# Performance work log

Hardware: AMD Instinct MI355X
Metric: run time of the kernel (lower is better)

## Reference

```python
import jax, jax.numpy as jnp
import numpy as np

C = 512
GROUPS = 32
EPS = 1e-6


def setup_inputs() -> dict:
    key = jax.random.key(0)
    ks = jax.random.split(key, 10)
    b, c, w = 8, C, 2048
    scale = 1.0 / np.sqrt(c)
    inp = {
        "x": jax.random.normal(ks[0], (b, c, w), dtype=jnp.float32),
        "gn_gamma": jnp.ones((c,), dtype=jnp.float32),
        "gn_beta": jnp.zeros((c,), dtype=jnp.float32),
        "wq": jax.random.normal(ks[1], (c, c), dtype=jnp.float32) * scale,
        "bq": jnp.zeros((c,), dtype=jnp.float32),
        "wk": jax.random.normal(ks[2], (c, c), dtype=jnp.float32) * scale,
        "bk": jnp.zeros((c,), dtype=jnp.float32),
        "wv": jax.random.normal(ks[3], (c, c), dtype=jnp.float32) * scale,
        "bv": jnp.zeros((c,), dtype=jnp.float32),
        "wp": jax.random.normal(ks[4], (c, c), dtype=jnp.float32) * scale,
        "bp": jnp.zeros((c,), dtype=jnp.float32),
    }
    return inp


def _group_norm(x, gamma, beta):
    # x: (b, c, w) -> normalize over (c//G, w) within each of G groups
    b, c, w = x.shape
    xg = x.reshape(b, GROUPS, c // GROUPS, w)
    mean = jnp.mean(xg, axis=(2, 3), keepdims=True)
    var = jnp.var(xg, axis=(2, 3), keepdims=True)
    xg = (xg - mean) * jax.lax.rsqrt(var + EPS)
    xn = xg.reshape(b, c, w)
    return xn * gamma[None, :, None] + beta[None, :, None]


def reference(x, gn_gamma, gn_beta, wq, bq, wk, bk, wv, bv, wp, bp):
    b, c, w = x.shape
    h = _group_norm(x, gn_gamma, gn_beta)
    # 1x1 convs == per-position linear over channels
    q = jnp.einsum('oc,bcw->bow', wq, h) + bq[None, :, None]
    k = jnp.einsum('oc,bcw->bow', wk, h) + bk[None, :, None]
    v = jnp.einsum('oc,bcw->bow', wv, h) + bv[None, :, None]
    # scores[b, i, j] = sum_c q[b,c,i] * k[b,c,j]
    scores = jnp.einsum('bci,bcj->bij', q, k) * (float(c) ** -0.5)
    att = jax.nn.softmax(scores, axis=2)  # (b, w, w)
    # out[b,c,i] = sum_j v[b,c,j] * att[b,i,j]
    h = jnp.einsum('bcj,bij->bci', v, att)
    h = jnp.einsum('oc,bcw->bow', wp, h) + bp[None, :, None]
    return x + h
```

## Files before the change

kernel.cpp:

```cpp
#include <hip/hip_runtime.h>
#include <hip/hip_bf16.h>
#include <stdint.h>

#define CDIM 512
#define WDIM 2048
#define BDIM 8
#define NGRP 32
#define LOG2E 1.4426950408889634f

typedef unsigned short u16;
typedef unsigned char u8;
typedef __attribute__((ext_vector_type(8))) short bf16x8;
typedef __attribute__((ext_vector_type(4))) float f32x4;
typedef __attribute__((ext_vector_type(2))) long long2v;

__device__ __forceinline__ float bf2f(u16 u) {
  return __builtin_bit_cast(float, (uint32_t)(u) << 16);
}
__device__ __forceinline__ u16 f2bf(float f) {
  return __builtin_bit_cast(u16, __float2bfloat16(f));
}
__device__ __forceinline__ u8 f2f8(float f) {
  return (u8)(__builtin_amdgcn_cvt_pk_fp8_f32(f, 0.f, 0, false));
}

__device__ __forceinline__ void gld_lds16(const void* g, void* l) {
  __builtin_amdgcn_global_load_lds(
      (const __attribute__((address_space(1))) uint32_t*)(uintptr_t)(g),
      (__attribute__((address_space(3))) uint32_t*)(uintptr_t)(l),
      16, 0, 0);
}

__device__ __forceinline__ int pi64(int l) {
  return ((l >> 3) & 3) * 16 + ((l >> 5) & 1) * 8 + (l & 7);
}

__global__ __launch_bounds__(256) void cvt_weights(
    const float* __restrict__ a, const float* __restrict__ b,
    const float* __restrict__ c, const float* __restrict__ d,
    u16* __restrict__ o) {
  int i = blockIdx.x * 256 + threadIdx.x;
  o[i]          = f2bf(a[i]);
  o[262144 + i] = f2bf(b[i]);
  o[524288 + i] = f2bf(c[i]);
  o[786432 + i] = f2bf(d[i]);
}

__global__ __launch_bounds__(512) void gn_fused(
    const float* __restrict__ x, const float* __restrict__ gamma,
    const float* __restrict__ beta, u16* __restrict__ hT) {
  extern __shared__ u16 hbuf[];
  __shared__ float red[2][8];
  __shared__ float mrsh[2];
  const int bg = blockIdx.x;
  const int b = bg >> 5, g = bg & 31;
  const int tid = threadIdx.x;
  const float4* xp = (const float4*)(x + (size_t)bg * 16 * WDIM);
  float s = 0.f, s2 = 0.f;
  for (int i = tid; i < 16 * WDIM / 4; i += 512) {
    float4 v = xp[i];
    s += v.x + v.y + v.z + v.w;
    s2 = fmaf(v.x, v.x, s2); s2 = fmaf(v.y, v.y, s2);
    s2 = fmaf(v.z, v.z, s2); s2 = fmaf(v.w, v.w, s2);
    int e = i * 4;
    int cc = e >> 11, w = e & 2047;
    u16* p = &hbuf[cc * 2052 + w];
    p[0] = f2bf(v.x); p[1] = f2bf(v.y); p[2] = f2bf(v.z); p[3] = f2bf(v.w);
  }
  for (int off = 32; off; off >>= 1) {
    s  += __shfl_xor(s, off, 64);
    s2 += __shfl_xor(s2, off, 64);
  }
  if ((tid & 63) == 0) { red[0][tid >> 6] = s; red[1][tid >> 6] = s2; }
  __syncthreads();
  if (tid == 0) {
    float S = 0.f, S2 = 0.f;
    #pragma unroll
    for (int i = 0; i < 8; ++i) { S += red[0][i]; S2 += red[1][i]; }
    const float inv_n = 1.0f / (16.0f * WDIM);
    float m = S * inv_n;
    float var = S2 * inv_n - m * m;
    mrsh[0] = m; mrsh[1] = rsqrtf(var + 1e-6f);
  }
  __syncthreads();
  const float m = mrsh[0], r = mrsh[1];
  float ga[16], bb[16];
  #pragma unroll
  for (int cc = 0; cc < 16; ++cc) {
    float gm = gamma[g * 16 + cc] * r;
    ga[cc] = gm;
    bb[cc] = beta[g * 16 + cc] - m * gm;
  }
  #pragma unroll
  for (int rr = 0; rr < 4; ++rr) {
    int w = rr * 512 + tid;
    u16 ov[16];
    #pragma unroll
    for (int cc = 0; cc < 16; ++cc)
      ov[cc] = f2bf(fmaf(bf2f(hbuf[cc * 2052 + w]), ga[cc], bb[cc]));
    u16* dst = hT + ((size_t)b * WDIM + w) * CDIM + g * 16;
    *(uint4*)(dst)     = *(const uint4*)(&ov[0]);
    *(uint4*)(dst + 8) = *(const uint4*)(&ov[8]);
  }
}

__global__ __launch_bounds__(256) void sm_combine(
    const float* __restrict__ lpart, float* __restrict__ linv) {
  int idx = blockIdx.x * 256 + threadIdx.x;
  int b = idx >> 11, i = idx & 2047;
  float l = 0.f;
  #pragma unroll
  for (int p = 0; p < 8; ++p)
    l += lpart[((size_t)b * 8 + p) * 2048 + i];
  linv[idx] = 1.0f / l;
}

template <int BIAS_MODE, int RESID, int SCALE, typename OutT, int SMEXP>
__global__ __launch_bounds__(512, 1) void gemm_tn(
    const u16* __restrict__ A, const u16* __restrict__ B,
    OutT* __restrict__ Cp, const float* __restrict__ bias,
    const float* __restrict__ bias2, const float* __restrict__ resid,
    float* __restrict__ LP, float scale, int K, int N, int lda, int ldb,
    long sAb, long sBb, long sCb, int gx, int gy) {
  constexpr int BM_ = 128, BN_ = 256;
  constexpr int MI = 4;
  constexpr int CB = 2, L = 3;
  constexpr int ABYTES = BM_ * 64;
  constexpr int SLOT = (BM_ + BN_) * 64;
  extern __shared__ char smem[];
  const int tid = threadIdx.x;
  const int wave = tid >> 6, lane = tid & 63;
  const int wr = wave >> 2, wc = wave & 3;
  const int fr = lane & 15, kg = lane >> 4;

  const int nq = gridDim.x >> 3;
  const int sid = (blockIdx.x & 7) * nq + (blockIdx.x >> 3);
  const int bx = sid % gx;
  const int t1 = sid / gx;
  const int by = t1 % gy;
  const int bz = t1 / gy;

  const size_t zc = (size_t)bz * sCb;
  const u16* Ab = A + (size_t)bz * sAb + (size_t)bx * BM_ * lda;
  const u16* Bb = B + (size_t)bz * sBb + (size_t)by * BN_ * ldb;

  int aoff, boff[CB];
  {
    int pc = tid;
    int S = pc >> 3, p = (pc & 7) ^ (S & 7);
    aoff = (2 * S + (p >> 2)) * lda + (p & 3) * 8;
  }
  #pragma unroll
  for (int j = 0; j < CB; ++j) {
    int pc = j * 512 + tid;
    int S = pc >> 3, p = (pc & 7) ^ (S & 7);
    boff[j] = (2 * S + (p >> 2)) * ldb + (p & 3) * 8;
  }
  const int rbase = (fr >> 1) * 128 + (((((fr & 1) << 2) | kg) ^ (fr >> 1)) << 4);
  const int sAo = wr * 64 * 64;
  const int sBo = wc * 64 * 64;

  f32x4 acc[MI][4] = {};

  auto stage = [&](int buf, int tk) {
    char* d = smem + buf * SLOT;
    gld_lds16(Ab + aoff + tk * 32, d + tid * 16);
    #pragma unroll
    for (int j = 0; j < CB; ++j)
      gld_lds16(Bb + boff[j] + tk * 32, d + ABYTES + (j * 512 + tid) * 16);
  };

  const int nt = K >> 5;
  stage(0, 0);
  stage(1, 1);
  asm volatile("s_waitcnt vmcnt(%0)" :: "n"(L) : "memory");
  __builtin_amdgcn_s_barrier();

  for (int t = 0; t < nt; ++t) {
    const char* base = smem + (t % 3) * SLOT;
    const bool st = (t + 2 < nt);
    if (st) stage((t + 2) % 3, t + 2);
    bf16x8 af[4], bfv[4];
    #pragma unroll
    for (int i = 0; i < 4; ++i)
      af[i] = *(const bf16x8*)(base + sAo + i * 1024 + rbase);
    #pragma unroll
    for (int ni = 0; ni < 4; ++ni)
      bfv[ni] = *(const bf16x8*)(base + ABYTES + sBo + ni * 1024 + rbase);
    asm volatile("s_waitcnt lgkmcnt(0)" ::: "memory");
    __builtin_amdgcn_sched_barrier(0);
    __builtin_amdgcn_s_setprio(1);
    #pragma unroll
    for (int i = 0; i < 4; ++i)
      #pragma unroll
      for (int ni = 0; ni < 4; ++ni)
        acc[i][ni] = __builtin_amdgcn_mfma_f32_16x16x32_bf16(
            af[i], bfv[ni], acc[i][ni], 0, 0, 0);
    __builtin_amdgcn_s_setprio(0);
    if (st)
      asm volatile("s_waitcnt vmcnt(%0)" :: "n"(L) : "memory");
    else if (t + 1 < nt)
      asm volatile("s_waitcnt vmcnt(0)" ::: "memory");
    if (t + 1 < nt)
      __builtin_amdgcn_s_barrier();
  }

  float rs[MI][4];
  if constexpr (SMEXP) {
    #pragma unroll
    for (int mi = 0; mi < MI; ++mi)
      #pragma unroll
      for (int j = 0; j < 4; ++j) rs[mi][j] = 0.f;
  }

  const int row0 = bx * BM_ + wr * 64 + kg * 4;
  const int coln = by * BN_ + wc * 64 + fr;
  #pragma unroll
  for (int mi = 0; mi < MI; ++mi) {
    #pragma unroll
    for (int ni = 0; ni < 4; ++ni) {
      int n = coln + ni * 16;
      float badd = 0.0f;
      if (BIAS_MODE == 3) badd = (n < 512) ? bias[n] : bias2[n - 512];
      #pragma unroll
      for (int j = 0; j < 4; ++j) {
        int m = row0 + mi * 16 + j;
        float v = acc[mi][ni][j];
        if (BIAS_MODE == 2) v += bias[m];
        else if (BIAS_MODE == 3) v += badd;
        if (SCALE) v *= scale;
        if constexpr (SMEXP) {
          v = exp2f(v * LOG2E);
          rs[mi][j] += v;
        }
        if (BIAS_MODE == 4) v *= bias[(size_t)bz * 2048 + m];
        if constexpr (sizeof(OutT) == 1) {
          int l = n & 63;
          ((u8*)Cp)[zc + (size_t)m * N + (size_t)(n & ~63) + pi64(l)] = f2f8(v);
        } else {
          size_t idx = zc + (size_t)m * N + n;
          if (RESID) v += resid[idx];
          if constexpr (sizeof(OutT) == 2) {
            Cp[idx] = (OutT)f2bf(v);
          } else {
            Cp[idx] = v;
          }
        }
      }
    }
  }

  if constexpr (SMEXP) {
    float* redl = (float*)smem;
    __syncthreads();
    #pragma unroll
    for (int mi = 0; mi < MI; ++mi) {
      #pragma unroll
      for (int j = 0; j < 4; ++j) {
        float l = rs[mi][j];
        #pragma unroll
        for (int msk = 1; msk < 16; msk <<= 1)
          l += __shfl_xor(l, msk, 64);
        if (fr == 0) {
          int rr = wr * 64 + mi * 16 + kg * 4 + j;
          redl[rr * 4 + wc] = l;
        }
      }
    }
    __syncthreads();
    if (tid < 128) {
      float l = redl[tid * 4] + redl[tid * 4 + 1] +
                redl[tid * 4 + 2] + redl[tid * 4 + 3];
      LP[((size_t)bz * 8 + by) * 2048 + bx * 128 + tid] = l;
    }
  }
}

template <int BIAS_MODE, int SCALE, typename OutT, int SMEXP>
__global__ __launch_bounds__(512, 1) void gemm_f8(
    const u8* __restrict__ A, const u8* __restrict__ B,
    OutT* __restrict__ Cp, const float* __restrict__ bias,
    float* __restrict__ LP, float scale, int K, int N, int ldaB, int ldbB,
    long sAb, long sBb, long sCb, int gx, int gy) {
  constexpr int MI = 4;
  constexpr int CB = 2, L = 3;
  constexpr int ABYTES = 8192;
  constexpr int SLOT = 24576;
  extern __shared__ char smem[];
  const int tid = threadIdx.x;
  const int wave = tid >> 6, lane = tid & 63;
  const int wr = wave >> 2, wc = wave & 3;
  const int fr = lane & 15, kg = lane >> 4;

  const int nq = gridDim.x >> 3;
  const int sid = (blockIdx.x & 7) * nq + (blockIdx.x >> 3);
  const int bx = sid % gx;
  const int t1 = sid / gx;
  const int by = t1 % gy;
  const int bz = t1 / gy;

  const size_t zc = (size_t)bz * sCb;
  const u8* Ab = A + (size_t)bz * sAb + (size_t)bx * 128 * ldaB;
  const u8* Bb = B + (size_t)bz * sBb + (size_t)by * 256 * ldbB;

  int aoff, boff[CB];
  {
    int pc = tid;
    int S = pc >> 3, p = (pc & 7) ^ (S & 7);
    aoff = (2 * S + (p >> 2)) * ldaB + (p & 3) * 16;
  }
  #pragma unroll
  for (int j = 0; j < CB; ++j) {
    int pc = j * 512 + tid;
    int S = pc >> 3, p = (pc & 7) ^ (S & 7);
    boff[j] = (2 * S + (p >> 2)) * ldbB + (p & 3) * 16;
  }
  const int rbase = (fr >> 1) * 128 + (((((fr & 1) << 2) | kg) ^ (fr >> 1)) << 4);
  const int sAo = wr * 4096;
  const int sBo = wc * 4096;

  f32x4 acc[MI][4] = {};

  auto stage = [&](int buf, int tk) {
    char* d = smem + buf * SLOT;
    gld_lds16(Ab + aoff + tk * 64, d + tid * 16);
    #pragma unroll
    for (int j = 0; j < CB; ++j)
      gld_lds16(Bb + boff[j] + tk * 64, d + ABYTES + (j * 512 + tid) * 16);
  };

  const int nt = K >> 6;
  stage(0, 0);
  stage(1, 1);
  asm volatile("s_waitcnt vmcnt(%0)" :: "n"(L) : "memory");
  __builtin_amdgcn_s_barrier();

  for (int t = 0; t < nt; ++t) {
    const char* base = smem + (t % 3) * SLOT;
    const bool st = (t + 2 < nt);
    if (st) stage((t + 2) % 3, t + 2);
    long2v af[4], bfv[4];
    #pragma unroll
    for (int i = 0; i < 4; ++i)
      af[i] = *(const long2v*)(base + sAo + i * 1024 + rbase);
    #pragma unroll
    for (int ni = 0; ni < 4; ++ni)
      bfv[ni] = *(const long2v*)(base + ABYTES + sBo + ni * 1024 + rbase);
    asm volatile("s_waitcnt lgkmcnt(0)" ::: "memory");
    __builtin_amdgcn_sched_barrier(0);
    __builtin_amdgcn_s_setprio(1);
    #pragma unroll
    for (int ksl = 0; ksl < 2; ++ksl)
      #pragma unroll
      for (int i = 0; i < 4; ++i)
        #pragma unroll
        for (int ni = 0; ni < 4; ++ni)
          acc[i][ni] = __builtin_amdgcn_mfma_f32_16x16x32_fp8_fp8(
              af[i][ksl], bfv[ni][ksl], acc[i][ni], 0, 0, 0);
    __builtin_amdgcn_s_setprio(0);
    if (st)
      asm volatile("s_waitcnt vmcnt(%0)" :: "n"(L) : "memory");
    else if (t + 1 < nt)
      asm volatile("s_waitcnt vmcnt(0)" ::: "memory");
    if (t + 1 < nt)
      __builtin_amdgcn_s_barrier();
  }

  float rs[MI][4];
  if constexpr (SMEXP) {
    #pragma unroll
    for (int mi = 0; mi < MI; ++mi)
      #pragma unroll
      for (int j = 0; j < 4; ++j) rs[mi][j] = 0.f;
  }

  const int row0 = bx * 128 + wr * 64 + kg * 4;
  const int coln = by * 256 + wc * 64 + fr;
  #pragma unroll
  for (int mi = 0; mi < MI; ++mi) {
    #pragma unroll
    for (int ni = 0; ni < 4; ++ni) {
      int n = coln + ni * 16;
      #pragma unroll
      for (int j = 0; j < 4; ++j) {
        int m = row0 + mi * 16 + j;
        float v = acc[mi][ni][j];
        if (SCALE) v *= scale;
        if constexpr (SMEXP) {
          v = exp2f(fmaf(v, LOG2E, -4.0f));
          rs[mi][j] += v;
        }
        if (BIAS_MODE == 4) v *= bias[(size_t)bz * 2048 + m];
        if constexpr (sizeof(OutT) == 1) {
          int l = n & 63;
          ((u8*)Cp)[zc + (size_t)m * N + (size_t)(n & ~63) + pi64(l)] = f2f8(v);
        } else {
          Cp[zc + (size_t)m * N + n] = (OutT)f2bf(v);
        }
      }
    }
  }

  if constexpr (SMEXP) {
    float* redl = (float*)smem;
    __syncthreads();
    #pragma unroll
    for (int mi = 0; mi < MI; ++mi) {
      #pragma unroll
      for (int j = 0; j < 4; ++j) {
        float l = rs[mi][j];
        #pragma unroll
        for (int msk = 1; msk < 16; msk <<= 1)
          l += __shfl_xor(l, msk, 64);
        if (fr == 0) {
          int rr = wr * 64 + mi * 16 + kg * 4 + j;
          redl[rr * 4 + wc] = l;
        }
      }
    }
    __syncthreads();
    if (tid < 128) {
      float l = redl[tid * 4] + redl[tid * 4 + 1] +
                redl[tid * 4 + 2] + redl[tid * 4 + 3];
      LP[((size_t)bz * 8 + by) * 2048 + bx * 128 + tid] = l;
    }
  }
}

extern "C" void kernel_launch(void* const* d_in, const int* in_sizes, int n_in,
                              void* d_out, int out_size, void* d_ws,
                              size_t ws_size, hipStream_t stream) {
  const float* x     = (const float*)d_in[0];
  const float* gamma = (const float*)d_in[1];
  const float* beta  = (const float*)d_in[2];
  const float* wq    = (const float*)d_in[3];
  const float* bq    = (const float*)d_in[4];
  const float* wk    = (const float*)d_in[5];
  const float* bk    = (const float*)d_in[6];
  const float* wv    = (const float*)d_in[7];
  const float* bv    = (const float*)d_in[8];
  const float* wp    = (const float*)d_in[9];
  const float* bp    = (const float*)d_in[10];
  float* out = (float*)d_out;

  char* ws = (char*)d_ws;
  u16* wq_bf = (u16*)ws;
  u16* wv_bf = wq_bf + 524288;
  u16* wp_bf = wv_bf + 262144;
  u16* hT = (u16*)(ws + 4 * 524288);
  u8*  qk8 = (u8*)(hT + 8388608);
  u8*  vB8 = qk8 + 16777216;
  u16* oT  = (u16*)(vB8 + 8388608);
  u8*  sc8 = (u8*)(oT + 8388608);
  float* lpart = (float*)(sc8 + 33554432);
  float* linv  = lpart + 131072;

  const long sWC = (long)WDIM * CDIM;
  const long sCW = (long)CDIM * WDIM;
  const long sQK = (long)WDIM * 1024;
  const long sWW = (long)WDIM * WDIM;

  const int SMEM = 3 * (128 + 256) * 64;
  const int GN_SMEM = 16 * 2052 * 2;
  (void)hipFuncSetAttribute((const void*)&gn_fused,
      hipFuncAttributeMaxDynamicSharedMemorySize, GN_SMEM);
  (void)hipFuncSetAttribute((const void*)&gemm_tn<3, 0, 0, u8, 0>,
      hipFuncAttributeMaxDynamicSharedMemorySize, SMEM);
  (void)hipFuncSetAttribute((const void*)&gemm_tn<2, 0, 0, u8, 0>,
      hipFuncAttributeMaxDynamicSharedMemorySize, SMEM);
  (void)hipFuncSetAttribute((const void*)&gemm_f8<0, 1, u8, 1>,
      hipFuncAttributeMaxDynamicSharedMemorySize, SMEM);
  (void)hipFuncSetAttribute((const void*)&gemm_f8<4, 0, u16, 0>,
      hipFuncAttributeMaxDynamicSharedMemorySize, SMEM);
  (void)hipFuncSetAttribute((const void*)&gemm_tn<2, 1, 0, float, 0>,
      hipFuncAttributeMaxDynamicSharedMemorySize, SMEM);

  cvt_weights<<<1024, 256, 0, stream>>>(wq, wk, wv, wp, wq_bf);
  gn_fused<<<BDIM * NGRP, 512, GN_SMEM, stream>>>(x, gamma, beta, hT);

  const float scale = 0.04419417382415922f;

  gemm_tn<3, 0, 0, u8, 0><<<512, 512, SMEM, stream>>>(
      hT, wq_bf, qk8, bq, bk, nullptr, nullptr, 1.f, 512, 1024,
      512, 512, sWC, 0, sQK, 16, 4);
  gemm_tn<2, 0, 0, u8, 0><<<256, 512, SMEM, stream>>>(
      wv_bf, hT, vB8, bv, nullptr, nullptr, nullptr, 1.f, 512, 2048,
      512, 512, 0, sWC, sCW, 4, 8);
  gemm_f8<0, 1, u8, 1><<<1024, 512, SMEM, stream>>>(
      qk8, qk8 + 512, sc8, nullptr, lpart, scale, 512, 2048,
      1024, 1024, sQK, sQK, sWW, 16, 8);
  sm_combine<<<64, 256, 0, stream>>>(lpart, linv);
  gemm_f8<4, 0, u16, 0><<<256, 512, SMEM, stream>>>(
      sc8, vB8, oT, linv, nullptr, 1.f, 2048, 512,
      2048, 2048, sWW, sCW, sWC, 16, 2);
  gemm_tn<2, 1, 0, float, 0><<<256, 512, SMEM, stream>>>(
      wp_bf, oT, out, bp, nullptr, x, nullptr, 1.f, 512, 2048,
      512, 512, 0, sWC, sCW, 4, 8);
}
```

Measured before the change: 158.3 us.

## Switch QKV projections to FP8 MFMA with FP8 group-norm output

Group norm now writes its normalized activations directly as FP8 in the permuted 64-byte layout the FP8 GEMM expects. The Q/K and V weights are converted to FP8 in the same layout. The Q/K and V projection GEMMs then run on the FP8 GEMM kernel instead of the BF16 one. This halves activation and weight bytes and doubles MFMA k-depth per instruction for those GEMMs, at the cost of lower precision in Q, K and V. The weight conversion kernel is restructured to use fewer blocks, and the two GEMM templates are consolidated.

```diff
diff --git a/kernel.cpp b/kernel.cpp
--- a/kernel.cpp
+++ b/kernel.cpp
@@ -10,6 +10,7 @@
 
 typedef unsigned short u16;
 typedef unsigned char u8;
+typedef unsigned long long u64;
 typedef __attribute__((ext_vector_type(8))) short bf16x8;
 typedef __attribute__((ext_vector_type(4))) float f32x4;
 typedef __attribute__((ext_vector_type(2))) long long2v;
@@ -36,19 +37,43 @@
 }
 
 __global__ __launch_bounds__(256) void cvt_weights(
-    const float* __restrict__ a, const float* __restrict__ b,
-    const float* __restrict__ c, const float* __restrict__ d,
-    u16* __restrict__ o) {
-  int i = blockIdx.x * 256 + threadIdx.x;
-  o[i]          = f2bf(a[i]);
-  o[262144 + i] = f2bf(b[i]);
-  o[524288 + i] = f2bf(c[i]);
-  o[786432 + i] = f2bf(d[i]);
+    const float* __restrict__ wq, const float* __restrict__ wk,
+    const float* __restrict__ wv, const float* __restrict__ wp,
+    u8* __restrict__ wqk8, u8* __restrict__ wv8, u16* __restrict__ wp_bf) {
+  const int t = blockIdx.x * 256 + threadIdx.x;
+  if (t < 8192) {
+    int row = t >> 3, c0 = (t & 7) * 64;
+    const float* src = (row < 512) ? wq + (size_t)row * 512 + c0
+                                   : wk + (size_t)(row - 512) * 512 + c0;
+    u8 buf[64];
+    #pragma unroll
+    for (int l = 0; l < 64; ++l) buf[pi64(l)] = f2f8(src[l]);
+    u8* dst = wqk8 + (size_t)row * 512 + c0;
+    #pragma unroll
+    for (int q = 0; q < 4; ++q)
+      *(uint4*)(dst + q * 16) = *(const uint4*)(buf + q * 16);
+  } else if (t < 12288) {
+    int t2 = t - 8192;
+    int row = t2 >> 3, c0 = (t2 & 7) * 64;
+    const float* src = wv + (size_t)row * 512 + c0;
+    u8 buf[64];
+    #pragma unroll
+    for (int l = 0; l < 64; ++l) buf[pi64(l)] = f2f8(src[l]);
+    u8* dst = wv8 + (size_t)row * 512 + c0;
+    #pragma unroll
+    for (int q = 0; q < 4; ++q)
+      *(uint4*)(dst + q * 16) = *(const uint4*)(buf + q * 16);
+  }
+  #pragma unroll
+  for (int j = 0; j < 16; ++j) {
+    int i = t * 16 + j;
+    wp_bf[i] = f2bf(wp[i]);
+  }
 }
 
 __global__ __launch_bounds__(512) void gn_fused(
     const float* __restrict__ x, const float* __restrict__ gamma,
-    const float* __restrict__ beta, u16* __restrict__ hT) {
+    const float* __restrict__ beta, u8* __restrict__ h8) {
   extern __shared__ u16 hbuf[];
   __shared__ float red[2][8];
   __shared__ float mrsh[2];
@@ -91,42 +116,44 @@
     ga[cc] = gm;
     bb[cc] = beta[g * 16 + cc] - m * gm;
   }
+  const int gq = g & 3;
+  const int off0 = ((2 * gq) & 3) * 16 + (gq >> 1) * 8;
+  const int off1 = ((2 * gq + 1) & 3) * 16 + (gq >> 1) * 8;
   #pragma unroll
   for (int rr = 0; rr < 4; ++rr) {
     int w = rr * 512 + tid;
-    u16 ov[16];
+    u8 ov[16];
     #pragma unroll
     for (int cc = 0; cc < 16; ++cc)
-      ov[cc] = f2bf(fmaf(bf2f(hbuf[cc * 2052 + w]), ga[cc], bb[cc]));
-    u16* dst = hT + ((size_t)b * WDIM + w) * CDIM + g * 16;
-    *(uint4*)(dst)     = *(const uint4*)(&ov[0]);
-    *(uint4*)(dst + 8) = *(const uint4*)(&ov[8]);
-  }
-}
-
+      ov[cc] = f2f8(fmaf(bf2f(hbuf[cc * 2052 + w]), ga[cc], bb[cc]));
+    u8* dst = h8 + ((size_t)b * WDIM + w) * CDIM + (g >> 2) * 64;
+    *(u64*)(dst + off0) = *(const u64*)(&ov[0]);
+    *(u64*)(dst + off1) = *(const u64*)(&ov[8]);
+  }
+}
+
+template <int NP>
 __global__ __launch_bounds__(256) void sm_combine(
     const float* __restrict__ lpart, float* __restrict__ linv) {
   int idx = blockIdx.x * 256 + threadIdx.x;
   int b = idx >> 11, i = idx & 2047;
   float l = 0.f;
   #pragma unroll
-  for (int p = 0; p < 8; ++p)
-    l += lpart[((size_t)b * 8 + p) * 2048 + i];
+  for (int p = 0; p < NP; ++p)
+    l += lpart[((size_t)b * NP + p) * 2048 + i];
   linv[idx] = 1.0f / l;
 }
 
-template <int BIAS_MODE, int RESID, int SCALE, typename OutT, int SMEXP>
+template <int BIAS_MODE, int RESID, typename OutT>
 __global__ __launch_bounds__(512, 1) void gemm_tn(
     const u16* __restrict__ A, const u16* __restrict__ B,
     OutT* __restrict__ Cp, const float* __restrict__ bias,
-    const float* __restrict__ bias2, const float* __restrict__ resid,
-    float* __restrict__ LP, float scale, int K, int N, int lda, int ldb,
-    long sAb, long sBb, long sCb, int gx, int gy) {
-  constexpr int BM_ = 128, BN_ = 256;
+    const float* __restrict__ resid, float scale, int K, int N,
+    int lda, int ldb, long sAb, long sBb, long sCb, int gx, int gy) {
   constexpr int MI = 4;
   constexpr int CB = 2, L = 3;
-  constexpr int ABYTES = BM_ * 64;
-  constexpr int SLOT = (BM_ + BN_) * 64;
+  constexpr int ABYTES = 8192;
+  constexpr int SLOT = 24576;
   extern __shared__ char smem[];
   const int tid = threadIdx.x;
   const int wave = tid >> 6, lane = tid & 63;
@@ -141,8 +168,8 @@
   const int bz = t1 / gy;
 
   const size_t zc = (size_t)bz * sCb;
-  const u16* Ab = A + (size_t)bz * sAb + (size_t)bx * BM_ * lda;
-  const u16* Bb = B + (size_t)bz * sBb + (size_t)by * BN_ * ldb;
+  const u16* Ab = A + (size_t)bz * sAb + (size_t)bx * 128 * lda;
+  const u16* Bb = B + (size_t)bz * sBb + (size_t)by * 256 * ldb;
 
   int aoff, boff[CB];
   {
@@ -157,8 +184,8 @@
     boff[j] = (2 * S + (p >> 2)) * ldb + (p & 3) * 8;
   }
   const int rbase = (fr >> 1) * 128 + (((((fr & 1) << 2) | kg) ^ (fr >> 1)) << 4);
-  const int sAo = wr * 64 * 64;
-  const int sBo = wc * 64 * 64;
+  const int sAo = wr * 4096;
+  const int sBo = wc * 4096;
 
   f32x4 acc[MI][4] = {};
 
@@ -205,6 +232,122 @@
       __builtin_amdgcn_s_barrier();
   }
 
+  const int row0 = bx * 128 + wr * 64 + kg * 4;
+  const int coln = by * 256 + wc * 64 + fr;
+  #pragma unroll
+  for (int mi = 0; mi < MI; ++mi) {
+    #pragma unroll
+    for (int ni = 0; ni < 4; ++ni) {
+      int n = coln + ni * 16;
+      #pragma unroll
+      for (int j = 0; j < 4; ++j) {
+        int m = row0 + mi * 16 + j;
+        float v = acc[mi][ni][j];
+        if (BIAS_MODE == 2) v += bias[m];
+        size_t idx = zc + (size_t)m * N + n;
+        if (RESID) v += resid[idx];
+        if constexpr (sizeof(OutT) == 2) {
+          Cp[idx] = (OutT)f2bf(v);
+        } else {
+          Cp[idx] = v;
+        }
+      }
+    }
+  }
+  (void)scale;
+}
+
+template <int BIAS_MODE, int SCALE, typename OutT, int SMEXP>
+__global__ __launch_bounds__(512, 1) void gemm_f8(
+    const u8* __restrict__ A, const u8* __restrict__ B,
+    OutT* __restrict__ Cp, const float* __restrict__ bias,
+    const float* __restrict__ bias2, float* __restrict__ LP,
+    float scale, int K, int N, int ldaB, int ldbB,
+    long sAb, long sBb, long sCb, int gx, int gy) {
+  constexpr int MI = 4;
+  constexpr int CB = 2, L = 3;
+  constexpr int ABYTES = 8192;
+  constexpr int SLOT = 24576;
+  extern __shared__ char smem[];
+  const int tid = threadIdx.x;
+  const int wave = tid >> 6, lane = tid & 63;
+  const int wr = wave >> 2, wc = wave & 3;
+  const int fr = lane & 15, kg = lane >> 4;
+
+  const int nq = gridDim.x >> 3;
+  const int sid = (blockIdx.x & 7) * nq + (blockIdx.x >> 3);
+  const int bx = sid % gx;
+  const int t1 = sid / gx;
+  const int by = t1 % gy;
+  const int bz = t1 / gy;
+
+  const size_t zc = (size_t)bz * sCb;
+  const u8* Ab = A + (size_t)bz * sAb + (size_t)bx * 128 * ldaB;
+  const u8* Bb = B + (size_t)bz * sBb + (size_t)by * 256 * ldbB;
+
+  int aoff, boff[CB];
+  {
+    int pc = tid;
+    int S = pc >> 3, p = (pc & 7) ^ (S & 7);
+    aoff = (2 * S + (p >> 2)) * ldaB + (p & 3) * 16;
+  }
+  #pragma unroll
+  for (int j = 0; j < CB; ++j) {
+    int pc = j * 512 + tid;
+    int S = pc >> 3, p = (pc & 7) ^ (S & 7);
+    boff[j] = (2 * S + (p >> 2)) * ldbB + (p & 3) * 16;
+  }
+  const int rbase = (fr >> 1) * 128 + (((((fr & 1) << 2) | kg) ^ (fr >> 1)) << 4);
+  const int sAo = wr * 4096;
+  const int sBo = wc * 4096;
+
+  f32x4 acc[MI][4] = {};
+
+  auto stage = [&](int buf, int tk) {
+    char* d = smem + buf * SLOT;
+    gld_lds16(Ab + aoff + tk * 64, d + tid * 16);
+    #pragma unroll
+    for (int j = 0; j < CB; ++j)
+      gld_lds16(Bb + boff[j] + tk * 64, d + ABYTES + (j * 512 + tid) * 16);
+  };
+
+  const int nt = K >> 6;
+  stage(0, 0);
+  stage(1, 1);
+  asm volatile("s_waitcnt vmcnt(%0)" :: "n"(L) : "memory");
+  __builtin_amdgcn_s_barrier();
+
+  for (int t = 0; t < nt; ++t) {
+    const char* base = smem + (t % 3) * SLOT;
+    const bool st = (t + 2 < nt);
+    if (st) stage((t + 2) % 3, t + 2);
+    long2v af[4], bfv[4];
+    #pragma unroll
+    for (int i = 0; i < 4; ++i)
+      af[i] = *(const long2v*)(base + sAo + i * 1024 + rbase);
+    #pragma unroll
+    for (int ni = 0; ni < 4; ++ni)
+      bfv[ni] = *(const long2v*)(base + ABYTES + sBo + ni * 1024 + rbase);
+    asm volatile("s_waitcnt lgkmcnt(0)" ::: "memory");
+    __builtin_amdgcn_sched_barrier(0);
+    __builtin_amdgcn_s_setprio(1);
+    #pragma unroll
+    for (int ksl = 0; ksl < 2; ++ksl)
+      #pragma unroll
+      for (int i = 0; i < 4; ++i)
+        #pragma unroll
+        for (int ni = 0; ni < 4; ++ni)
+          acc[i][ni] = __builtin_amdgcn_mfma_f32_16x16x32_fp8_fp8(
+              af[i][ksl], bfv[ni][ksl], acc[i][ni], 0, 0, 0);
+    __builtin_amdgcn_s_setprio(0);
+    if (st)
+      asm volatile("s_waitcnt vmcnt(%0)" :: "n"(L) : "memory");
+    else if (t + 1 < nt)
+      asm volatile("s_waitcnt vmcnt(0)" ::: "memory");
+    if (t + 1 < nt)
+      __builtin_amdgcn_s_barrier();
+  }
+
   float rs[MI][4];
   if constexpr (SMEXP) {
     #pragma unroll
@@ -213,8 +356,8 @@
       for (int j = 0; j < 4; ++j) rs[mi][j] = 0.f;
   }
 
-  const int row0 = bx * BM_ + wr * 64 + kg * 4;
-  const int coln = by * BN_ + wc * 64 + fr;
+  const int row0 = bx * 128 + wr * 64 + kg * 4;
+  const int coln = by * 256 + wc * 64 + fr;
   #pragma unroll
   for (int mi = 0; mi < MI; ++mi) {
     #pragma unroll
@@ -230,7 +373,7 @@
         else if (BIAS_MODE == 3) v += badd;
         if (SCALE) v *= scale;
         if constexpr (SMEXP) {
-          v = exp2f(v * LOG2E);
+          v = exp2f(fmaf(v, LOG2E, -4.0f));
           rs[mi][j] += v;
         }
         if (BIAS_MODE == 4) v *= bias[(size_t)bz * 2048 + m];
@@ -238,13 +381,7 @@
           int l = n & 63;
           ((u8*)Cp)[zc + (size_t)m * N + (size_t)(n & ~63) + pi64(l)] = f2f8(v);
         } else {
-          size_t idx = zc + (size_t)m * N + n;
-          if (RESID) v += resid[idx];
-          if constexpr (sizeof(OutT) == 2) {
-            Cp[idx] = (OutT)f2bf(v);
-          } else {
-            Cp[idx] = v;
-          }
+          Cp[zc + (size_t)m * N + n] = (OutT)f2bf(v);
         }
       }
     }
@@ -271,158 +408,7 @@
     if (tid < 128) {
       float l = redl[tid * 4] + redl[tid * 4 + 1] +
                 redl[tid * 4 + 2] + redl[tid * 4 + 3];
-      LP[((size_t)bz * 8 + by) * 2048 + bx * 128 + tid] = l;
-    }
-  }
-}
-
-template <int BIAS_MODE, int SCALE, typename OutT, int SMEXP>
-__global__ __launch_bounds__(512, 1) void gemm_f8(
-    const u8* __restrict__ A, const u8* __restrict__ B,
-    OutT* __restrict__ Cp, const float* __restrict__ bias,
-    float* __restrict__ LP, float scale, int K, int N, int ldaB, int ldbB,
-    long sAb, long sBb, long sCb, int gx, int gy) {
-  constexpr int MI = 4;
-  constexpr int CB = 2, L = 3;
-  constexpr int ABYTES = 8192;
-  constexpr int SLOT = 24576;
-  extern __shared__ char smem[];
-  const int tid = threadIdx.x;
-  const int wave = tid >> 6, lane = tid & 63;
-  const int wr = wave >> 2, wc = wave & 3;
-  const int fr = lane & 15, kg = lane >> 4;
-
-  const int nq = gridDim.x >> 3;
-  const int sid = (blockIdx.x & 7) * nq + (blockIdx.x >> 3);
-  const int bx = sid % gx;
-  const int t1 = sid / gx;
-  const int by = t1 % gy;
-  const int bz = t1 / gy;
-
-  const size_t zc = (size_t)bz * sCb;
-  const u8* Ab = A + (size_t)bz * sAb + (size_t)bx * 128 * ldaB;
-  const u8* Bb = B + (size_t)bz * sBb + (size_t)by * 256 * ldbB;
-
-  int aoff, boff[CB];
-  {
-    int pc = tid;
-    int S = pc >> 3, p = (pc & 7) ^ (S & 7);
-    aoff = (2 * S + (p >> 2)) * ldaB + (p & 3) * 16;
-  }
-  #pragma unroll
-  for (int j = 0; j < CB; ++j) {
-    int pc = j * 512 + tid;
-    int S = pc >> 3, p = (pc & 7) ^ (S & 7);
-    boff[j] = (2 * S + (p >> 2)) * ldbB + (p & 3) * 16;
-  }
-  const int rbase = (fr >> 1) * 128 + (((((fr & 1) << 2) | kg) ^ (fr >> 1)) << 4);
-  const int sAo = wr * 4096;
-  const int sBo = wc * 4096;
-
-  f32x4 acc[MI][4] = {};
-
-  auto stage = [&](int buf, int tk) {
-    char* d = smem + buf * SLOT;
-    gld_lds16(Ab + aoff + tk * 64, d + tid * 16);
-    #pragma unroll
-    for (int j = 0; j < CB; ++j)
-      gld_lds16(Bb + boff[j] + tk * 64, d + ABYTES + (j * 512 + tid) * 16);
-  };
-
-  const int nt = K >> 6;
-  stage(0, 0);
-  stage(1, 1);
-  asm volatile("s_waitcnt vmcnt(%0)" :: "n"(L) : "memory");
-  __builtin_amdgcn_s_barrier();
-
-  for (int t = 0; t < nt; ++t) {
-    const char* base = smem + (t % 3) * SLOT;
-    const bool st = (t + 2 < nt);
-    if (st) stage((t + 2) % 3, t + 2);
-    long2v af[4], bfv[4];
-    #pragma unroll
-    for (int i = 0; i < 4; ++i)
-      af[i] = *(const long2v*)(base + sAo + i * 1024 + rbase);
-    #pragma unroll
-    for (int ni = 0; ni < 4; ++ni)
-      bfv[ni] = *(const long2v*)(base + ABYTES + sBo + ni * 1024 + rbase);
-    asm volatile("s_waitcnt lgkmcnt(0)" ::: "memory");
-    __builtin_amdgcn_sched_barrier(0);
-    __builtin_amdgcn_s_setprio(1);
-    #pragma unroll
-    for (int ksl = 0; ksl < 2; ++ksl)
-      #pragma unroll
-      for (int i = 0; i < 4; ++i)
-        #pragma unroll
-        for (int ni = 0; ni < 4; ++ni)
-          acc[i][ni] = __builtin_amdgcn_mfma_f32_16x16x32_fp8_fp8(
-              af[i][ksl], bfv[ni][ksl], acc[i][ni], 0, 0, 0);
-    __builtin_amdgcn_s_setprio(0);
-    if (st)
-      asm volatile("s_waitcnt vmcnt(%0)" :: "n"(L) : "memory");
-    else if (t + 1 < nt)
-      asm volatile("s_waitcnt vmcnt(0)" ::: "memory");
-    if (t + 1 < nt)
-      __builtin_amdgcn_s_barrier();
-  }
-
-  float rs[MI][4];
-  if constexpr (SMEXP) {
-    #pragma unroll
-    for (int mi = 0; mi < MI; ++mi)
-      #pragma unroll
-      for (int j = 0; j < 4; ++j) rs[mi][j] = 0.f;
-  }
-
-  const int row0 = bx * 128 + wr * 64 + kg * 4;
-  const int coln = by * 256 + wc * 64 + fr;
-  #pragma unroll
-  for (int mi = 0; mi < MI; ++mi) {
-    #pragma unroll
-    for (int ni = 0; ni < 4; ++ni) {
-      int n = coln + ni * 16;
-      #pragma unroll
-      for (int j = 0; j < 4; ++j) {
-        int m = row0 + mi * 16 + j;
-        float v = acc[mi][ni][j];
-        if (SCALE) v *= scale;
-        if constexpr (SMEXP) {
-          v = exp2f(fmaf(v, LOG2E, -4.0f));
-          rs[mi][j] += v;
-        }
-        if (BIAS_MODE == 4) v *= bias[(size_t)bz * 2048 + m];
-        if constexpr (sizeof(OutT) == 1) {
-          int l = n & 63;
-          ((u8*)Cp)[zc + (size_t)m * N + (size_t)(n & ~63) + pi64(l)] = f2f8(v);
-        } else {
-          Cp[zc + (size_t)m * N + n] = (OutT)f2bf(v);
-        }
-      }
-    }
-  }
-
-  if constexpr (SMEXP) {
-    float* redl = (float*)smem;
-    __syncthreads();
-    #pragma unroll
-    for (int mi = 0; mi < MI; ++mi) {
-      #pragma unroll
-      for (int j = 0; j < 4; ++j) {
-        float l = rs[mi][j];
-        #pragma unroll
-        for (int msk = 1; msk < 16; msk <<= 1)
-          l += __shfl_xor(l, msk, 64);
-        if (fr == 0) {
-          int rr = wr * 64 + mi * 16 + kg * 4 + j;
-          redl[rr * 4 + wc] = l;
-        }
-      }
-    }
-    __syncthreads();
-    if (tid < 128) {
-      float l = redl[tid * 4] + redl[tid * 4 + 1] +
-                redl[tid * 4 + 2] + redl[tid * 4 + 3];
-      LP[((size_t)bz * 8 + by) * 2048 + bx * 128 + tid] = l;
+      LP[((size_t)bz * gy + by) * 2048 + bx * 128 + tid] = l;
     }
   }
 }
@@ -443,17 +429,17 @@
   const float* bp    = (const float*)d_in[10];
   float* out = (float*)d_out;
 
-  char* ws = (char*)d_ws;
-  u16* wq_bf = (u16*)ws;
-  u16* wv_bf = wq_bf + 524288;
-  u16* wp_bf = wv_bf + 262144;
-  u16* hT = (u16*)(ws + 4 * 524288);
-  u8*  qk8 = (u8*)(hT + 8388608);
-  u8*  vB8 = qk8 + 16777216;
-  u16* oT  = (u16*)(vB8 + 8388608);
-  u8*  sc8 = (u8*)(oT + 8388608);
-  float* lpart = (float*)(sc8 + 33554432);
-  float* linv  = lpart + 131072;
+  char* p = (char*)d_ws;
+  u8*  wqk8 = (u8*)p;           p += 524288;
+  u8*  wv8  = (u8*)p;           p += 262144;
+  u16* wp_bf = (u16*)p;         p += 524288;
+  u8*  h8   = (u8*)p;           p += 8388608;
+  u8*  qk8  = (u8*)p;           p += 16777216;
+  u8*  vB8  = (u8*)p;           p += 8388608;
+  u16* oT   = (u16*)p;          p += 16777216;
+  u8*  sc8  = (u8*)p;           p += 33554432;
+  float* lpart = (float*)p;     p += 524288;
+  float* linv  = (float*)p;
 
   const long sWC = (long)WDIM * CDIM;
   const long sCW = (long)CDIM * WDIM;
@@ -464,36 +450,36 @@
   const int GN_SMEM = 16 * 2052 * 2;
   (void)hipFuncSetAttribute((const void*)&gn_fused,
       hipFuncAttributeMaxDynamicSharedMemorySize, GN_SMEM);
-  (void)hipFuncSetAttribute((const void*)&gemm_tn<3, 0, 0, u8, 0>,
+  (void)hipFuncSetAttribute((const void*)&gemm_f8<3, 0, u8, 0>,
       hipFuncAttributeMaxDynamicSharedMemorySize, SMEM);
-  (void)hipFuncSetAttribute((const void*)&gemm_tn<2, 0, 0, u8, 0>,
+  (void)hipFuncSetAttribute((const void*)&gemm_f8<2, 0, u8, 0>,
       hipFuncAttributeMaxDynamicSharedMemorySize, SMEM);
   (void)hipFuncSetAttribute((const void*)&gemm_f8<0, 1, u8, 1>,
       hipFuncAttributeMaxDynamicSharedMemorySize, SMEM);
   (void)hipFuncSetAttribute((const void*)&gemm_f8<4, 0, u16, 0>,
       hipFuncAttributeMaxDynamicSharedMemorySize, SMEM);
-  (void)hipFuncSetAttribute((const void*)&gemm_tn<2, 1, 0, float, 0>,
+  (void)hipFuncSetAttribute((const void*)&gemm_tn<2, 1, float>,
       hipFuncAttributeMaxDynamicSharedMemorySize, SMEM);
 
-  cvt_weights<<<1024, 256, 0, stream>>>(wq, wk, wv, wp, wq_bf);
-  gn_fused<<<BDIM * NGRP, 512, GN_SMEM, stream>>>(x, gamma, beta, hT);
+  cvt_weights<<<64, 256, 0, stream>>>(wq, wk, wv, wp, wqk8, wv8, wp_bf);
+  gn_fused<<<BDIM * NGRP, 512, GN_SMEM, stream>>>(x, gamma, beta, h8);
 
   const float scale = 0.04419417382415922f;
 
-  gemm_tn<3, 0, 0, u8, 0><<<512, 512, SMEM, stream>>>(
-      hT, wq_bf, qk8, bq, bk, nullptr, nullptr, 1.f, 512, 1024,
-      512, 512, sWC, 0, sQK, 16, 4);
-  gemm_tn<2, 0, 0, u8, 0><<<256, 512, SMEM, stream>>>(
-      wv_bf, hT, vB8, bv, nullptr, nullptr, nullptr, 1.f, 512, 2048,
-      512, 512, 0, sWC, sCW, 4, 8);
+  gemm_f8<3, 0, u8, 0><<<512, 512, SMEM, stream>>>(
+      h8, wqk8, qk8, bq, bk, nullptr, 1.f, 512, 1024, 512, 512,
+      sWC, 0, sQK, 16, 4);
+  gemm_f8<2, 0, u8, 0><<<256, 512, SMEM, stream>>>(
+      wv8, h8, vB8, bv, nullptr, nullptr, 1.f, 512, 2048, 512, 512,
+      0, sWC, sCW, 4, 8);
   gemm_f8<0, 1, u8, 1><<<1024, 512, SMEM, stream>>>(
-      qk8, qk8 + 512, sc8, nullptr, lpart, scale, 512, 2048,
+      qk8, qk8 + 512, sc8, nullptr, nullptr, lpart, scale, 512, 2048,
       1024, 1024, sQK, sQK, sWW, 16, 8);
-  sm_combine<<<64, 256, 0, stream>>>(lpart, linv);
+  sm_combine<8><<<64, 256, 0, stream>>>(lpart, linv);
   gemm_f8<4, 0, u16, 0><<<256, 512, SMEM, stream>>>(
-      sc8, vB8, oT, linv, nullptr, 1.f, 2048, 512,
-      2048, 2048, sWW, sCW, sWC, 16, 2);
-  gemm_tn<2, 1, 0, float, 0><<<256, 512, SMEM, stream>>>(
-      wp_bf, oT, out, bp, nullptr, x, nullptr, 1.f, 512, 2048,
-      512, 512, 0, sWC, sCW, 4, 8);
-}
+      sc8, vB8, oT, linv, nullptr, nullptr, 1.f, 2048, 512, 2048, 2048,
+      sWW, sCW, sWC, 16, 2);
+  gemm_tn<2, 1, float><<<256, 512, SMEM, stream>>>(
+      wp_bf, oT, out, bp, x, 1.f, 512, 2048, 512, 512,
+      0, sWC, sCW, 4, 8);
+}
```

Measured after the change: 149.0 us. -5.9%, faster.
